# Kernel optimization log

Hardware: AMD Instinct MI355X
Metric: run time of the kernel (lower is better)

Reference implementation:

```python
import jax, jax.numpy as jnp
import numpy as np


def setup_inputs() -> dict:
    key = jax.random.key(0)
    k1, k2 = jax.random.split(key)
    B, C, H, W = 8, 128, 96, 160
    x1 = jax.random.normal(k1, (B, C, H, W), dtype=jnp.float32)
    x2 = jax.random.normal(k2, (B, C, H, W), dtype=jnp.float32)
    return {"x1": x1, "x2": x2, "d": 4}


def reference(x1, x2, d):
    # x1, x2: (B, C, H, W); output: (B, (2d+1)^2, H, W)
    b, c, h, w = x1.shape
    x2p = jnp.pad(x2, ((0, 0), (0, 0), (d, d), (d, d)))
    # Loop over the small fixed (2d+1)^2 displacement set (81 for d=4);
    # each term is a channel-reduced elementwise product (shift-multiply-sum).
    corrs = [
        jnp.einsum("bchw,bchw->bhw", x1,
                   jax.lax.dynamic_slice(x2p, (0, 0, i, j), (b, c, h, w)))
        for i in range(2 * d + 1)
        for j in range(2 * d + 1)
    ]
    out = jnp.stack(corrs, axis=1)  # (B, (2d+1)^2, H, W)
    return out / c
```

## Files before the change

kernel.cpp:

```cpp
#include <hip/hip_runtime.h>
#include <stdint.h>
#include <stddef.h>

#define Bb 8
#define Cc 128
#define Hh 96
#define Ww 160
#define HW (Hh*Ww)
#define Kk 81

typedef __attribute__((ext_vector_type(8))) short short8;
typedef __attribute__((ext_vector_type(4))) float floatx4;
typedef __attribute__((ext_vector_type(4))) unsigned int uintx4;

__device__ __forceinline__ uint32_t bf16rne(float f) {
  uint32_t u = __float_as_uint(f);
  return (u + 0x7FFFu + ((u >> 16) & 1u)) >> 16;
}

#define SBAR() __builtin_amdgcn_sched_barrier(0)


#define TPXF 1024
__global__ __launch_bounds__(256, 8)
void transpose_kernel(const float* __restrict__ x2, ushort* __restrict__ x2t) {
  const int t   = threadIdx.x;
  const int b   = blockIdx.y;
  const int px0 = blockIdx.x * TPXF;
  const int cg  = blockIdx.z;

  const float* sb = x2 + (size_t)(b * Cc + cg * 8) * HW + px0 + t * 4;
  floatx4 v0 = *(const floatx4*)(sb + (size_t)0 * HW);
  floatx4 v1 = *(const floatx4*)(sb + (size_t)1 * HW);
  floatx4 v2 = *(const floatx4*)(sb + (size_t)2 * HW);
  floatx4 v3 = *(const floatx4*)(sb + (size_t)3 * HW);
  floatx4 v4 = *(const floatx4*)(sb + (size_t)4 * HW);
  floatx4 v5 = *(const floatx4*)(sb + (size_t)5 * HW);
  floatx4 v6 = *(const floatx4*)(sb + (size_t)6 * HW);
  floatx4 v7 = *(const floatx4*)(sb + (size_t)7 * HW);
  SBAR();

  ushort* dbase = x2t + (((size_t)b * 16 + cg) * HW + px0 + t * 4) * 8;
#pragma unroll
  for (int j = 0; j < 4; ++j) {
    uintx4 q = (uintx4){bf16rne(v0[j]) | (bf16rne(v1[j]) << 16),
                        bf16rne(v2[j]) | (bf16rne(v3[j]) << 16),
                        bf16rne(v4[j]) | (bf16rne(v5[j]) << 16),
                        bf16rne(v6[j]) | (bf16rne(v7[j]) << 16)};
    *(uintx4*)&dbase[(size_t)j * 8] = q;
  }
}

__device__ __forceinline__ int clampi(int v, int lo, int hi) {
  return v < lo ? lo : (v > hi ? hi : v);
}

#define CKSTEP ((long)4 * HW * 8)
#define X1STR 136

#define LOADRAW(dst, tt, ckc)                                                  \
  dst = *(const short8*)&base2c[rowoff##tt + (ckc) * CKSTEP];

#define ZSEL(v, tt)                                                            \
  v = (okw && (unsigned)(gh2b + (tt)) < (unsigned)Hh) ? v                      \
      : (short8){0, 0, 0, 0, 0, 0, 0, 0};

__global__ __launch_bounds__(256, 3)
void corr_t4_kernel(const float* __restrict__ x1, const ushort* __restrict__ x2t,
                    float* __restrict__ out) {
  __shared__ float  ldsOut[Kk * 66];
  __shared__ ushort ldsX1[64 * X1STR];

  const int tid  = threadIdx.x;
  const int flat = blockIdx.x;
  const int b  = flat & 7;
  const int j  = flat >> 3;
  const int by = j / 10;
  const int bx = j - by * 10;
  const int w0 = bx * 16;
  const int h0 = by * 4;

  const int lane = tid & 63;
  const int wv   = tid >> 6;
  const int vy = wv & 1, vx = wv >> 1;
  const int n = lane & 15, quad = lane >> 4;
  const int s = n >> 3, pw = n & 7;

  {
    const float* x1base = x1 + (size_t)(b * Cc) * HW + (size_t)h0 * Ww + w0;
#pragma unroll
    for (int it = 0; it < 8; ++it) {
      int T   = it * 256 + tid;
      int c   = T >> 4;
      int rem = T & 15;
      int r   = rem >> 2;
      int q4  = rem & 3;
      floatx4 v = *(const floatx4*)&x1base[(size_t)c * HW + r * Ww + q4 * 4];
      int px = r * 16 + q4 * 4;
#pragma unroll
      for (int jj = 0; jj < 4; ++jj)
        ldsX1[(px + jj) * X1STR + c] = (ushort)bf16rne(v[jj]);
    }
  }

  floatx4 acc[10];
#pragma unroll
  for (int t = 0; t < 10; ++t) acc[t] = (floatx4){0.f, 0.f, 0.f, 0.f};

  const int gw2  = w0 - 4 + 8 * vx + n;
  const bool okw = (unsigned)gw2 < (unsigned)Ww;
  const int gw2c = clampi(gw2, 0, Ww - 1);
  const int gh2b = h0 - 4 + 2 * vy;

  const ushort* base2c = x2t + (((long)b * 16 + quad) * HW + gw2c) * 8;

  const long rowoff0 = (long)clampi(gh2b + 0, 0, Hh - 1) * (Ww * 8);
  const long rowoff1 = (long)clampi(gh2b + 1, 0, Hh - 1) * (Ww * 8);
  const long rowoff2 = (long)clampi(gh2b + 2, 0, Hh - 1) * (Ww * 8);
  const long rowoff3 = (long)clampi(gh2b + 3, 0, Hh - 1) * (Ww * 8);
  const long rowoff4 = (long)clampi(gh2b + 4, 0, Hh - 1) * (Ww * 8);
  const long rowoff5 = (long)clampi(gh2b + 5, 0, Hh - 1) * (Ww * 8);
  const long rowoff6 = (long)clampi(gh2b + 6, 0, Hh - 1) * (Ww * 8);
  const long rowoff7 = (long)clampi(gh2b + 7, 0, Hh - 1) * (Ww * 8);
  const long rowoff8 = (long)clampi(gh2b + 8, 0, Hh - 1) * (Ww * 8);
  const long rowoff9 = (long)clampi(gh2b + 9, 0, Hh - 1) * (Ww * 8);

  short8 aA0, aA1, aA2, aA3, aA4, aA5, aA6, aA7, aA8, aA9;
  short8 aB0, aB1, aB2, aB3, aB4, aB5, aB6, aB7, aB8, aB9;

  LOADRAW(aA0, 0, 0); LOADRAW(aA1, 1, 0); LOADRAW(aA2, 2, 0); LOADRAW(aA3, 3, 0);
  LOADRAW(aA4, 4, 0); LOADRAW(aA5, 5, 0); LOADRAW(aA6, 6, 0); LOADRAW(aA7, 7, 0);
  LOADRAW(aA8, 8, 0); LOADRAW(aA9, 9, 0);
  SBAR();
  LOADRAW(aB0, 0, 1); LOADRAW(aB1, 1, 1); LOADRAW(aB2, 2, 1); LOADRAW(aB3, 3, 1);
  LOADRAW(aB4, 4, 1); LOADRAW(aB5, 5, 1); LOADRAW(aB6, 6, 1); LOADRAW(aB7, 7, 1);
  LOADRAW(aB8, 8, 1); LOADRAW(aB9, 9, 1);
  SBAR();

  __syncthreads();
  const int pxl = (2 * vy + s) * 16 + 8 * vx + pw;
  const short8 bf0 = *(const short8*)&ldsX1[pxl * X1STR +  0 + quad * 8];
  const short8 bf1 = *(const short8*)&ldsX1[pxl * X1STR + 32 + quad * 8];
  const short8 bf2 = *(const short8*)&ldsX1[pxl * X1STR + 64 + quad * 8];
  const short8 bf3 = *(const short8*)&ldsX1[pxl * X1STR + 96 + quad * 8];
  SBAR();

  ZSEL(aA0, 0); ZSEL(aA1, 1); ZSEL(aA2, 2); ZSEL(aA3, 3); ZSEL(aA4, 4);
  ZSEL(aA5, 5); ZSEL(aA6, 6); ZSEL(aA7, 7); ZSEL(aA8, 8); ZSEL(aA9, 9);
  acc[0] = __builtin_amdgcn_mfma_f32_16x16x32_bf16(aA0, bf0, acc[0], 0, 0, 0);
  acc[1] = __builtin_amdgcn_mfma_f32_16x16x32_bf16(aA1, bf0, acc[1], 0, 0, 0);
  acc[2] = __builtin_amdgcn_mfma_f32_16x16x32_bf16(aA2, bf0, acc[2], 0, 0, 0);
  acc[3] = __builtin_amdgcn_mfma_f32_16x16x32_bf16(aA3, bf0, acc[3], 0, 0, 0);
  acc[4] = __builtin_amdgcn_mfma_f32_16x16x32_bf16(aA4, bf0, acc[4], 0, 0, 0);
  acc[5] = __builtin_amdgcn_mfma_f32_16x16x32_bf16(aA5, bf0, acc[5], 0, 0, 0);
  acc[6] = __builtin_amdgcn_mfma_f32_16x16x32_bf16(aA6, bf0, acc[6], 0, 0, 0);
  acc[7] = __builtin_amdgcn_mfma_f32_16x16x32_bf16(aA7, bf0, acc[7], 0, 0, 0);
  acc[8] = __builtin_amdgcn_mfma_f32_16x16x32_bf16(aA8, bf0, acc[8], 0, 0, 0);
  acc[9] = __builtin_amdgcn_mfma_f32_16x16x32_bf16(aA9, bf0, acc[9], 0, 0, 0);
  SBAR();
  LOADRAW(aA0, 0, 2); LOADRAW(aA1, 1, 2); LOADRAW(aA2, 2, 2); LOADRAW(aA3, 3, 2);
  LOADRAW(aA4, 4, 2); LOADRAW(aA5, 5, 2); LOADRAW(aA6, 6, 2); LOADRAW(aA7, 7, 2);
  LOADRAW(aA8, 8, 2); LOADRAW(aA9, 9, 2);
  SBAR();
  ZSEL(aB0, 0); ZSEL(aB1, 1); ZSEL(aB2, 2); ZSEL(aB3, 3); ZSEL(aB4, 4);
  ZSEL(aB5, 5); ZSEL(aB6, 6); ZSEL(aB7, 7); ZSEL(aB8, 8); ZSEL(aB9, 9);
  acc[0] = __builtin_amdgcn_mfma_f32_16x16x32_bf16(aB0, bf1, acc[0], 0, 0, 0);
  acc[1] = __builtin_amdgcn_mfma_f32_16x16x32_bf16(aB1, bf1, acc[1], 0, 0, 0);
  acc[2] = __builtin_amdgcn_mfma_f32_16x16x32_bf16(aB2, bf1, acc[2], 0, 0, 0);
  acc[3] = __builtin_amdgcn_mfma_f32_16x16x32_bf16(aB3, bf1, acc[3], 0, 0, 0);
  acc[4] = __builtin_amdgcn_mfma_f32_16x16x32_bf16(aB4, bf1, acc[4], 0, 0, 0);
  acc[5] = __builtin_amdgcn_mfma_f32_16x16x32_bf16(aB5, bf1, acc[5], 0, 0, 0);
  acc[6] = __builtin_amdgcn_mfma_f32_16x16x32_bf16(aB6, bf1, acc[6], 0, 0, 0);
  acc[7] = __builtin_amdgcn_mfma_f32_16x16x32_bf16(aB7, bf1, acc[7], 0, 0, 0);
  acc[8] = __builtin_amdgcn_mfma_f32_16x16x32_bf16(aB8, bf1, acc[8], 0, 0, 0);
  acc[9] = __builtin_amdgcn_mfma_f32_16x16x32_bf16(aB9, bf1, acc[9], 0, 0, 0);
  SBAR();
  LOADRAW(aB0, 0, 3); LOADRAW(aB1, 1, 3); LOADRAW(aB2, 2, 3); LOADRAW(aB3, 3, 3);
  LOADRAW(aB4, 4, 3); LOADRAW(aB5, 5, 3); LOADRAW(aB6, 6, 3); LOADRAW(aB7, 7, 3);
  LOADRAW(aB8, 8, 3); LOADRAW(aB9, 9, 3);
  SBAR();
  ZSEL(aA0, 0); ZSEL(aA1, 1); ZSEL(aA2, 2); ZSEL(aA3, 3); ZSEL(aA4, 4);
  ZSEL(aA5, 5); ZSEL(aA6, 6); ZSEL(aA7, 7); ZSEL(aA8, 8); ZSEL(aA9, 9);
  acc[0] = __builtin_amdgcn_mfma_f32_16x16x32_bf16(aA0, bf2, acc[0], 0, 0, 0);
  acc[1] = __builtin_amdgcn_mfma_f32_16x16x32_bf16(aA1, bf2, acc[1], 0, 0, 0);
  acc[2] = __builtin_amdgcn_mfma_f32_16x16x32_bf16(aA2, bf2, acc[2], 0, 0, 0);
  acc[3] = __builtin_amdgcn_mfma_f32_16x16x32_bf16(aA3, bf2, acc[3], 0, 0, 0);
  acc[4] = __builtin_amdgcn_mfma_f32_16x16x32_bf16(aA4, bf2, acc[4], 0, 0, 0);
  acc[5] = __builtin_amdgcn_mfma_f32_16x16x32_bf16(aA5, bf2, acc[5], 0, 0, 0);
  acc[6] = __builtin_amdgcn_mfma_f32_16x16x32_bf16(aA6, bf2, acc[6], 0, 0, 0);
  acc[7] = __builtin_amdgcn_mfma_f32_16x16x32_bf16(aA7, bf2, acc[7], 0, 0, 0);
  acc[8] = __builtin_amdgcn_mfma_f32_16x16x32_bf16(aA8, bf2, acc[8], 0, 0, 0);
  acc[9] = __builtin_amdgcn_mfma_f32_16x16x32_bf16(aA9, bf2, acc[9], 0, 0, 0);
  SBAR();
  ZSEL(aB0, 0); ZSEL(aB1, 1); ZSEL(aB2, 2); ZSEL(aB3, 3); ZSEL(aB4, 4);
  ZSEL(aB5, 5); ZSEL(aB6, 6); ZSEL(aB7, 7); ZSEL(aB8, 8); ZSEL(aB9, 9);
  acc[0] = __builtin_amdgcn_mfma_f32_16x16x32_bf16(aB0, bf3, acc[0], 0, 0, 0);
  acc[1] = __builtin_amdgcn_mfma_f32_16x16x32_bf16(aB1, bf3, acc[1], 0, 0, 0);
  acc[2] = __builtin_amdgcn_mfma_f32_16x16x32_bf16(aB2, bf3, acc[2], 0, 0, 0);
  acc[3] = __builtin_amdgcn_mfma_f32_16x16x32_bf16(aB3, bf3, acc[3], 0, 0, 0);
  acc[4] = __builtin_amdgcn_mfma_f32_16x16x32_bf16(aB4, bf3, acc[4], 0, 0, 0);
  acc[5] = __builtin_amdgcn_mfma_f32_16x16x32_bf16(aB5, bf3, acc[5], 0, 0, 0);
  acc[6] = __builtin_amdgcn_mfma_f32_16x16x32_bf16(aB6, bf3, acc[6], 0, 0, 0);
  acc[7] = __builtin_amdgcn_mfma_f32_16x16x32_bf16(aB7, bf3, acc[7], 0, 0, 0);
  acc[8] = __builtin_amdgcn_mfma_f32_16x16x32_bf16(aB8, bf3, acc[8], 0, 0, 0);
  acc[9] = __builtin_amdgcn_mfma_f32_16x16x32_bf16(aB9, bf3, acc[9], 0, 0, 0);

  const float scale = 1.0f / 128.0f;
  const int prow = 2 * vy + s;
  const int pcol = 8 * vx + pw;
#pragma unroll
  for (int t = 0; t < 10; ++t) {
    int di = t - 4 - s;
    if ((unsigned)(di + 4) > 8u) continue;
#pragma unroll
    for (int r = 0; r < 4; ++r) {
      int dj = quad * 4 + r - 4 - pw;
      if ((unsigned)(dj + 4) > 8u) continue;
      int kk = (di + 4) * 9 + (dj + 4);
      ldsOut[kk * 66 + prow * 16 + pcol] = acc[t][r] * scale;
    }
  }
  __syncthreads();

  for (int idx = tid; idx < Kk * 64; idx += 256) {
    int kk  = idx >> 6;
    int rem = idx & 63;
    int hh  = rem >> 4;
    int ww  = rem & 15;
    out[((size_t)b * Kk + kk) * HW + (size_t)(h0 + hh) * Ww + (w0 + ww)] =
        ldsOut[kk * 66 + rem];
  }
}

__global__ __launch_bounds__(512, 4)
void corr_kernel(const float* __restrict__ x1, const float* __restrict__ x2,
                 float* __restrict__ out) {
  __shared__ __align__(16) ushort ldsX2[16*24*40];
  __shared__ __align__(16) ushort ldsX1f[8*16*40];

  const int tid = threadIdx.x;
  const int flat = blockIdx.x;
  const int b  = flat & 7;
  const int j  = flat >> 3;
  const int by = j / 10;
  const int bx = j - by * 10;
  const int w0 = bx * 16;
  const int h0 = by * 8;

  const int lane = tid & 63;
  const int wv   = tid >> 6;
  const int vy = wv & 3, vx = wv >> 2;
  const int n = lane & 15, quad = lane >> 4;
  const int s = n >> 3, pw = n & 7;

  floatx4 acc[10];
#pragma unroll
  for (int t = 0; t < 10; ++t) acc[t] = (floatx4){0.f, 0.f, 0.f, 0.f};

  for (int ck = 0; ck < 4; ++ck) {
    const int c0 = ck * 32;
    if (ck) __syncthreads();

#pragma unroll
    for (int it = 0; it < 3; ++it) {
      int T   = it * 512 + tid;
      int w24 = T % 24;
      int t2  = T / 24;
      int rw  = t2 & 15;
      int cg  = t2 >> 4;
      int gh = h0 - 4 + rw;
      int gw = w0 - 4 + w24;
      bool ok = ((unsigned)gh < Hh) && ((unsigned)gw < Ww);
      const float* src = x2 + ((size_t)(b*Cc + c0 + cg*8) * HW + gh*Ww + gw);
      uint32_t p0, p1, p2, p3;
      {
        float a0 = ok ? src[0*HW] : 0.f;
        float a1 = ok ? src[1*HW] : 0.f;
        float a2 = ok ? src[2*HW] : 0.f;
        float a3 = ok ? src[3*HW] : 0.f;
        float a4 = ok ? src[4*HW] : 0.f;
        float a5 = ok ? src[5*HW] : 0.f;
        float a6 = ok ? src[6*HW] : 0.f;
        float a7 = ok ? src[7*HW] : 0.f;
        p0 = bf16rne(a0) | (bf16rne(a1) << 16);
        p1 = bf16rne(a2) | (bf16rne(a3) << 16);
        p2 = bf16rne(a4) | (bf16rne(a5) << 16);
        p3 = bf16rne(a6) | (bf16rne(a7) << 16);
      }
      *(uintx4*)&ldsX2[(rw*24 + w24)*40 + cg*8] = (uintx4){p0, p1, p2, p3};
    }

    {
      int T  = tid;
      int wl = T & 15;
      int t2 = T >> 4;
      int rl = t2 & 7;
      int cg = t2 >> 3;
      const float* src = x1 + ((size_t)(b*Cc + c0 + cg*8) * HW
                               + (h0 + rl)*Ww + (w0 + wl));
      uint32_t p0, p1, p2, p3;
      float a0 = src[0*HW], a1 = src[1*HW], a2 = src[2*HW], a3 = src[3*HW];
      float a4 = src[4*HW], a5 = src[5*HW], a6 = src[6*HW], a7 = src[7*HW];
      p0 = bf16rne(a0) | (bf16rne(a1) << 16);
      p1 = bf16rne(a2) | (bf16rne(a3) << 16);
      p2 = bf16rne(a4) | (bf16rne(a5) << 16);
      p3 = bf16rne(a6) | (bf16rne(a7) << 16);
      *(uintx4*)&ldsX1f[(rl*16 + wl)*40 + cg*8] = (uintx4){p0, p1, p2, p3};
    }

    __syncthreads();

    short8 bfrag = *(const short8*)&ldsX1f[((2*vy + s)*16 + 8*vx + pw)*40 + quad*8];
#pragma unroll
    for (int t = 0; t < 10; ++t) {
      short8 afrag = *(const short8*)&ldsX2[((2*vy + t)*24 + 8*vx + n)*40 + quad*8];
      acc[t] = __builtin_amdgcn_mfma_f32_16x16x32_bf16(afrag, bfrag, acc[t], 0, 0, 0);
    }
  }

  const float scale = 1.0f / 128.0f;
  const int ph  = h0 + 2*vy + s;
  const int pwg = w0 + 8*vx + pw;
#pragma unroll
  for (int t = 0; t < 10; ++t) {
    int di = t - 4 - s;
    if ((unsigned)(di + 4) > 8u) continue;
#pragma unroll
    for (int r = 0; r < 4; ++r) {
      int dj = quad*4 + r - 4 - pw;
      if ((unsigned)(dj + 4) > 8u) continue;
      int kk = (di + 4) * 9 + (dj + 4);
      out[((size_t)b*Kk + kk) * HW + ph*Ww + pwg] = acc[t][r] * scale;
    }
  }
}

extern "C" void kernel_launch(void* const* d_in, const int* in_sizes, int n_in,
                              void* d_out, int out_size, void* d_ws, size_t ws_size,
                              hipStream_t stream) {
  const float* x1 = (const float*)d_in[0];
  const float* x2 = (const float*)d_in[1];
  float* out = (float*)d_out;

  const size_t elems = (size_t)Bb * HW * Cc;
  const size_t need  = elems * sizeof(ushort);

  if (d_ws != nullptr && ws_size >= need) {
    ushort* x2t = (ushort*)d_ws;
    transpose_kernel<<<dim3(HW / TPXF, Bb, 16), dim3(256, 1, 1), 0, stream>>>(
        x2, x2t);
    corr_t4_kernel<<<dim3(1920, 1, 1), dim3(256, 1, 1), 0, stream>>>(x1, x2t, out);
  } else {
    corr_kernel<<<dim3(960, 1, 1), dim3(512, 1, 1), 0, stream>>>(x1, x2, out);
  }
}
```

Measured before the change: 185.6 us.

## Alias LDS buffers, vectorize x1 staging, and overlap x1 loads with x2 prefetch

The separate x1 and output LDS arrays become one aliased buffer, which lowers per-block LDS and may allow more resident blocks. Each thread now loads 8 channels of x1 into registers and issues those loads before the x2 prefetch. It then packs them to bf16 and writes one 16-byte vector per pixel instead of scalar ushort stores. An extra barrier after the x1 fragment reads protects the aliased buffer before the output stage reuses it.

```diff
diff --git a/kernel.cpp b/kernel.cpp
--- a/kernel.cpp
+++ b/kernel.cpp
@@ -66,10 +66,11 @@
       : (short8){0, 0, 0, 0, 0, 0, 0, 0};
 
 __global__ __launch_bounds__(256, 3)
-void corr_t4_kernel(const float* __restrict__ x1, const ushort* __restrict__ x2t,
+void corr_t5_kernel(const float* __restrict__ x1, const ushort* __restrict__ x2t,
                     float* __restrict__ out) {
-  __shared__ float  ldsOut[Kk * 66];
-  __shared__ ushort ldsX1[64 * X1STR];
+  __shared__ __align__(16) unsigned char ldsRaw[Kk * 66 * 4];
+  ushort* ldsX1  = (ushort*)ldsRaw;
+  float*  ldsOut = (float*)ldsRaw;
 
   const int tid  = threadIdx.x;
   const int flat = blockIdx.x;
@@ -86,26 +87,21 @@
   const int n = lane & 15, quad = lane >> 4;
   const int s = n >> 3, pw = n & 7;
 
-  {
-    const float* x1base = x1 + (size_t)(b * Cc) * HW + (size_t)h0 * Ww + w0;
-#pragma unroll
-    for (int it = 0; it < 8; ++it) {
-      int T   = it * 256 + tid;
-      int c   = T >> 4;
-      int rem = T & 15;
-      int r   = rem >> 2;
-      int q4  = rem & 3;
-      floatx4 v = *(const floatx4*)&x1base[(size_t)c * HW + r * Ww + q4 * 4];
-      int px = r * 16 + q4 * 4;
-#pragma unroll
-      for (int jj = 0; jj < 4; ++jj)
-        ldsX1[(px + jj) * X1STR + c] = (ushort)bf16rne(v[jj]);
-    }
-  }
-
-  floatx4 acc[10];
-#pragma unroll
-  for (int t = 0; t < 10; ++t) acc[t] = (floatx4){0.f, 0.f, 0.f, 0.f};
+  const int p   = tid & 15;
+  const int cgs = tid >> 4;
+  const int rs  = p >> 2;
+  const int ws4 = (p & 3) * 4;
+  const float* x1b = x1 + (size_t)(b * Cc + cgs * 8) * HW
+                        + (size_t)(h0 + rs) * Ww + w0 + ws4;
+  floatx4 u0 = *(const floatx4*)(x1b + (size_t)0 * HW);
+  floatx4 u1 = *(const floatx4*)(x1b + (size_t)1 * HW);
+  floatx4 u2 = *(const floatx4*)(x1b + (size_t)2 * HW);
+  floatx4 u3 = *(const floatx4*)(x1b + (size_t)3 * HW);
+  floatx4 u4 = *(const floatx4*)(x1b + (size_t)4 * HW);
+  floatx4 u5 = *(const floatx4*)(x1b + (size_t)5 * HW);
+  floatx4 u6 = *(const floatx4*)(x1b + (size_t)6 * HW);
+  floatx4 u7 = *(const floatx4*)(x1b + (size_t)7 * HW);
+  SBAR();
 
   const int gw2  = w0 - 4 + 8 * vx + n;
   const bool okw = (unsigned)gw2 < (unsigned)Ww;
@@ -137,13 +133,30 @@
   LOADRAW(aB8, 8, 1); LOADRAW(aB9, 9, 1);
   SBAR();
 
+  {
+    const int pxb = rs * 16 + ws4;
+#pragma unroll
+    for (int jj = 0; jj < 4; ++jj) {
+      uintx4 q = (uintx4){bf16rne(u0[jj]) | (bf16rne(u1[jj]) << 16),
+                          bf16rne(u2[jj]) | (bf16rne(u3[jj]) << 16),
+                          bf16rne(u4[jj]) | (bf16rne(u5[jj]) << 16),
+                          bf16rne(u6[jj]) | (bf16rne(u7[jj]) << 16)};
+      *(uintx4*)&ldsX1[(pxb + jj) * X1STR + cgs * 8] = q;
+    }
+  }
   __syncthreads();
+
   const int pxl = (2 * vy + s) * 16 + 8 * vx + pw;
   const short8 bf0 = *(const short8*)&ldsX1[pxl * X1STR +  0 + quad * 8];
   const short8 bf1 = *(const short8*)&ldsX1[pxl * X1STR + 32 + quad * 8];
   const short8 bf2 = *(const short8*)&ldsX1[pxl * X1STR + 64 + quad * 8];
   const short8 bf3 = *(const short8*)&ldsX1[pxl * X1STR + 96 + quad * 8];
-  SBAR();
+  __syncthreads();
+  SBAR();
+
+  floatx4 acc[10];
+#pragma unroll
+  for (int t = 0; t < 10; ++t) acc[t] = (floatx4){0.f, 0.f, 0.f, 0.f};
 
   ZSEL(aA0, 0); ZSEL(aA1, 1); ZSEL(aA2, 2); ZSEL(aA3, 3); ZSEL(aA4, 4);
   ZSEL(aA5, 5); ZSEL(aA6, 6); ZSEL(aA7, 7); ZSEL(aA8, 8); ZSEL(aA9, 9);
@@ -349,7 +362,7 @@
     ushort* x2t = (ushort*)d_ws;
     transpose_kernel<<<dim3(HW / TPXF, Bb, 16), dim3(256, 1, 1), 0, stream>>>(
         x2, x2t);
-    corr_t4_kernel<<<dim3(1920, 1, 1), dim3(256, 1, 1), 0, stream>>>(x1, x2t, out);
+    corr_t5_kernel<<<dim3(1920, 1, 1), dim3(256, 1, 1), 0, stream>>>(x1, x2t, out);
   } else {
     corr_kernel<<<dim3(960, 1, 1), dim3(512, 1, 1), 0, stream>>>(x1, x2, out);
   }
```

Measured after the change: 183.0 us. No clear change (-1.4%).
